# Performance work log

Measured on AMD Instinct MI355X. Metric: run time of the kernel, lower is better.

## Reference

```python
import jax, jax.numpy as jnp
import numpy as np

DIM = 256
WINDOW = 512  # look_backward=1, look_forward=0, causal


def setup_inputs() -> dict:
    key = jax.random.key(0)
    ks = jax.random.split(key, 7)
    B, N, D = 8, 8192, DIM
    s = D ** -0.5
    return {
        "x": jax.random.normal(ks[0], (B, D, N), dtype=jnp.float32),
        "Wq": jax.random.normal(ks[1], (D, D), dtype=jnp.float32) * s,
        "bq": jax.random.normal(ks[2], (D,), dtype=jnp.float32) * 0.01,
        "Wk": jax.random.normal(ks[3], (D, D), dtype=jnp.float32) * s,
        "bk": jax.random.normal(ks[4], (D,), dtype=jnp.float32) * 0.01,
        "Wv": jax.random.normal(ks[5], (D, D), dtype=jnp.float32) * s,
        "bv": jax.random.normal(ks[6], (D,), dtype=jnp.float32) * 0.01,
    }


def _local_attention(q, k, v, window):
    # q,k,v: (B, N, D); causal sliding-window attention, look_backward=1 window.
    b, n, d = q.shape
    nw = n // window  # N assumed multiple of window (autopad no-op here)
    scale = d ** -0.5
    qb = q.reshape(b, nw, window, d)
    kb = k.reshape(b, nw, window, d)
    vb = v.reshape(b, nw, window, d)

    def look_back(t):
        prev = jnp.pad(t, ((0, 0), (1, 0), (0, 0), (0, 0)))[:, :-1]
        return jnp.concatenate([prev, t], axis=2)  # (b, nw, 2*window, d)

    kb2 = look_back(kb)
    vb2 = look_back(vb)

    pos = jnp.arange(n).reshape(nw, window)
    prev_pos = jnp.pad(pos, ((1, 0), (0, 0)), constant_values=-1)[:-1]
    kpos = jnp.concatenate([prev_pos, pos], axis=1)  # (nw, 2*window)
    # causal mask + mask out the (nonexistent) window before window 0
    mask = (pos[:, :, None] >= kpos[:, None, :]) & (kpos[:, None, :] >= 0)

    scores = jnp.einsum('bnqd,bnkd->bnqk', qb, kb2) * scale
    scores = jnp.where(mask[None], scores, jnp.asarray(-1e9, scores.dtype))
    attn = jax.nn.softmax(scores, axis=-1)  # dropout(0.1) omitted: eval mode
    out = jnp.einsum('bnqk,bnkd->bnqd', attn, vb2)
    return out.reshape(b, n, d)


def reference(x, Wq, bq, Wk, bk, Wv, bv):
    # x: (B, D, N) -> permute -> (B, N, D)
    xp = jnp.transpose(x, (0, 2, 1))
    q = xp @ Wq.T + bq
    k = xp @ Wk.T + bk
    v = xp @ Wv.T + bv
    y = xp + _local_attention(q, k, v, WINDOW)  # residual
    return jnp.transpose(y, (0, 2, 1))
```

## Files before the change

kernel.cpp:

```cpp
#include <hip/hip_runtime.h>
#include <hip/hip_bf16.h>

#define DIM  256
#define NSEQ 8192
#define BATCH 8
#define WIN  512

typedef __attribute__((ext_vector_type(8))) short short8;
typedef __attribute__((ext_vector_type(4))) float floatx4;

union PFU { int i[4]; short8 v; };

__device__ __forceinline__ int packbf(float a, float b) {
    __hip_bfloat162 h;
    h.x = __float2bfloat16(a);
    h.y = __float2bfloat16(b);
    int r;
    __builtin_memcpy(&r, &h, 4);
    return r;
}

__global__ __launch_bounds__(256) void k_wcast(const float* __restrict__ w0,
                                               const float* __restrict__ w1,
                                               const float* __restrict__ w2,
                                               __hip_bfloat16* __restrict__ wb) {
    int i = (blockIdx.x * 256 + threadIdx.x) * 4;
    const float* s = (i < 65536) ? (w0 + i) : ((i < 131072) ? (w1 + i - 65536) : (w2 + i - 131072));
    float4 v = *(const float4*)s;
    union { __hip_bfloat16 h[4]; ushort4 u; } cv;
    cv.h[0] = __float2bfloat16(v.x);
    cv.h[1] = __float2bfloat16(v.y);
    cv.h[2] = __float2bfloat16(v.z);
    cv.h[3] = __float2bfloat16(v.w);
    *(ushort4*)(wb + i) = cv.u;
}

__global__ __launch_bounds__(256, 3) void k_prep(const float* __restrict__ x,
                                                 const __hip_bfloat16* __restrict__ wb,
                                                 const float* __restrict__ bq,
                                                 const float* __restrict__ bk,
                                                 const float* __restrict__ bv,
                                                 __hip_bfloat16* __restrict__ qo,
                                                 __hip_bfloat16* __restrict__ ko,
                                                 __hip_bfloat16* __restrict__ vto) {
    __shared__ float ftile[64][68];
    __shared__ __align__(16) char As[32768];
    const int b   = blockIdx.y;
    const int n0  = blockIdx.x * 64;
    const int tid = threadIdx.x;
    const int wv  = tid >> 6;
    const int l   = tid & 63;
    const int lm  = l & 15;
    const int qd  = l >> 4;
    const int wn  = wv * 64;

    const float* xb = x + (size_t)b * DIM * NSEQ;

    const int dr = l >> 4, nseg = l & 15;
#pragma unroll
    for (int dsl = 0; dsl < 4; ++dsl) {
        const int d0 = dsl * 64;
#pragma unroll
        for (int i = 0; i < 4; ++i) {
            const int r = wv * 16 + i * 4 + dr;
            float4 v = *(const float4*)(xb + (size_t)(d0 + r) * NSEQ + n0 + nseg * 4);
            *(float4*)&ftile[r][nseg * 4] = v;
        }
        __syncthreads();
#pragma unroll
        for (int p = 0; p < 2; ++p) {
            const int ks = dsl * 2 + p;
            int4 pk;
            int* pki = (int*)&pk;
#pragma unroll
            for (int jj = 0; jj < 4; ++jj)
                pki[jj] = packbf(ftile[p * 32 + wv * 8 + jj * 2][l],
                                 ftile[p * 32 + wv * 8 + jj * 2 + 1][l]);
            *(int4*)(As + ks * 4096 + wv * 1024 + l * 16) = pk;
        }
        __syncthreads();
    }

#pragma unroll
    for (int mode = 0; mode < 3; ++mode) {
        const __hip_bfloat16* wp = wb + mode * 65536;
        floatx4 acc[4][4];
#pragma unroll
        for (int i = 0; i < 4; ++i)
#pragma unroll
            for (int j = 0; j < 4; ++j) acc[i][j] = (floatx4){0.f, 0.f, 0.f, 0.f};

#pragma unroll
        for (int ks = 0; ks < 8; ++ks) {
            short8 wf[4], af[4];
#pragma unroll
            for (int j = 0; j < 4; ++j)
                wf[j] = *(const short8*)(wp + (size_t)(wn + j * 16 + lm) * DIM + ks * 32 + qd * 8);
#pragma unroll
            for (int j = 0; j < 4; ++j)
                af[j] = *(const short8*)(As + ks * 4096 + qd * 1024 + (j * 16 + lm) * 16);
            if (mode < 2) {
#pragma unroll
                for (int mt = 0; mt < 4; ++mt)
#pragma unroll
                    for (int nt = 0; nt < 4; ++nt)
                        acc[mt][nt] = __builtin_amdgcn_mfma_f32_16x16x32_bf16(af[mt], wf[nt], acc[mt][nt], 0, 0, 0);
            } else {
#pragma unroll
                for (int jw = 0; jw < 4; ++jw)
#pragma unroll
                    for (int ja = 0; ja < 4; ++ja)
                        acc[jw][ja] = __builtin_amdgcn_mfma_f32_16x16x32_bf16(wf[jw], af[ja], acc[jw][ja], 0, 0, 0);
            }
        }

        if (mode < 2) {
            const float* bias = mode ? bk : bq;
            __hip_bfloat16* op = (mode ? ko : qo) + (size_t)b * NSEQ * DIM;
            float bc[4];
#pragma unroll
            for (int nt = 0; nt < 4; ++nt) bc[nt] = bias[wn + nt * 16 + lm];
#pragma unroll
            for (int mt = 0; mt < 4; ++mt)
#pragma unroll
                for (int nt = 0; nt < 4; ++nt)
#pragma unroll
                    for (int r = 0; r < 4; ++r)
                        op[(size_t)(n0 + mt * 16 + qd * 4 + r) * DIM + wn + nt * 16 + lm] =
                            __float2bfloat16(acc[mt][nt][r] + bc[nt]);
        } else {
            __hip_bfloat16* op = vto + (size_t)b * DIM * NSEQ;
#pragma unroll
            for (int jw = 0; jw < 4; ++jw)
#pragma unroll
                for (int r = 0; r < 4; ++r) {
                    const int d = wn + jw * 16 + qd * 4 + r;
                    const float bb = bv[d];
#pragma unroll
                    for (int ja = 0; ja < 4; ++ja)
                        op[(size_t)d * NSEQ + n0 + ja * 16 + lm] =
                            __float2bfloat16(acc[jw][ja][r] + bb);
                }
        }
    }
}

__global__ __launch_bounds__(1024, 4) void k_attn(const __hip_bfloat16* __restrict__ qm,
                                                  const __hip_bfloat16* __restrict__ km,
                                                  const __hip_bfloat16* __restrict__ vtm,
                                                  const float* __restrict__ x,
                                                  float* __restrict__ out) {
    __shared__ __align__(16) char kbuf[2][16384];
    __shared__ __align__(16) char vbuf[2][16384];

    const int w  = blockIdx.x, b = blockIdx.y, qt = blockIdx.z;
    const int tid = threadIdx.x;
    const int wv = tid >> 6;
    const int l  = tid & 63;
    const int m  = l & 15;
    const int qd = l >> 4;

    const int qbw   = qt * 256 + wv * 16;
    const int koff0 = w * WIN - WIN;

    short8 qf[8];
    {
        const __hip_bfloat16* qrow =
            qm + ((size_t)b * NSEQ + (size_t)(w * WIN + qbw + m)) * DIM;
#pragma unroll
        for (int s = 0; s < 8; ++s)
            qf[s] = *(const short8*)(qrow + s * 32 + qd * 8);
    }

    const char* kbase = (const char*)(km + (size_t)b * NSEQ * DIM);
    const char* vbase = (const char*)(vtm + (size_t)b * DIM * NSEQ);

    const int c0  = (w == 0) ? 16 : 0;
    const int c1w = (512 + qbw + 47) >> 5;
    const int c1b = (799 + qt * 256) >> 5;

    const bool   isK = wv < 8;
    const int    wk  = wv & 7;
    const size_t gstride = isK ? (size_t)64 : (size_t)16 * NSEQ * 2;
    const size_t adv     = isK ? (size_t)32 * 512 : (size_t)64;
    const int    lbase   = wk * 2048 + l * 16;
    const char* gp0;
    if (isK)
        gp0 = kbase + (size_t)(koff0 + c0 * 32 + (wk >> 2) * 16 + m) * 512 +
              (size_t)(((wk >> 1) & 1) * 16 + qd) * 16 + (size_t)(wk & 1) * 128;
    else
        gp0 = vbase + (size_t)((wk >> 1) * 64 + (wk & 1) * 32 + m) * (NSEQ * 2) +
              (size_t)(koff0 + c0 * 32) * 2 + (size_t)qd * 16;

    floatx4 o[16];
#pragma unroll
    for (int t = 0; t < 16; ++t) o[t] = (floatx4){0.f, 0.f, 0.f, 0.f};
    float mi = -INFINITY;
    float li = 0.f;
    const float sscale = 0.0625f * 1.4426950408889634f;

    const int a0 = (((qd & 1) * 2) * 16 + m) * 4;
    const int a1 = a0 + 64;
    const bool hi = (qd >> 1) != 0;

    int4 rg[2];
#pragma unroll
    for (int i = 0; i < 2; ++i)
        rg[i] = *(const int4*)(gp0 + (size_t)i * gstride);
    gp0 += adv;
    {
        char* d0 = (isK ? kbuf[0] : vbuf[0]) + lbase;
#pragma unroll
        for (int i = 0; i < 2; ++i)
            *(int4*)(d0 + i * 1024) = rg[i];
    }
    __syncthreads();

    int pb = 0;
    for (int c = c0; c < c1b; ++c) {
        const bool more = (c + 1 < c1b);
        if (more) {
#pragma unroll
            for (int i = 0; i < 2; ++i)
                rg[i] = *(const int4*)(gp0 + (size_t)i * gstride);
            gp0 += adv;
        }
        if (c < c1w) {
            const char* kbp = kbuf[pb];
            floatx4 st[2];
            st[0] = (floatx4){0.f, 0.f, 0.f, 0.f};
            st[1] = (floatx4){0.f, 0.f, 0.f, 0.f};
            __builtin_amdgcn_s_setprio(1);
#pragma unroll
            for (int t = 0; t < 2; ++t)
#pragma unroll
                for (int s = 0; s < 8; ++s) {
                    short8 kf = *(const short8*)(kbp + ((t * 8 + s) * 64 + l) * 16);
                    st[t] = __builtin_amdgcn_mfma_f32_16x16x32_bf16(kf, qf[s], st[t], 0, 0, 0);
                }
            __builtin_amdgcn_s_setprio(0);
            const int kl0 = c * 32;
            const int lim = 512 + qbw + m;
            const bool needmask = (kl0 + 31) > lim;
            float p[8];
#pragma unroll
            for (int t = 0; t < 2; ++t)
#pragma unroll
                for (int r = 0; r < 4; ++r) {
                    float v = st[t][r] * sscale;
                    if (needmask) {
                        int key = kl0 + t * 16 + qd * 4 + r;
                        v = (key <= lim) ? v : -INFINITY;
                    }
                    p[t * 4 + r] = v;
                }
            float mx = p[0];
#pragma unroll
            for (int i = 1; i < 8; ++i) mx = fmaxf(mx, p[i]);
            mx = fmaxf(mx, __shfl_xor(mx, 16, 64));
            mx = fmaxf(mx, __shfl_xor(mx, 32, 64));
            float mnew;
            if (__all(mx <= mi + 8.0f)) mnew = mi;
            else                        mnew = fmaxf(mi, mx);
            const float alpha = exp2f(mi - mnew);
            float ps = 0.f;
#pragma unroll
            for (int i = 0; i < 8; ++i) { p[i] = exp2f(p[i] - mnew); ps += p[i]; }
            ps += __shfl_xor(ps, 16, 64);
            ps += __shfl_xor(ps, 32, 64);
            li = li * alpha + ps;
            mi = mnew;
            if (!__all(alpha == 1.0f)) {
#pragma unroll
                for (int t = 0; t < 16; ++t) {
                    o[t][0] *= alpha; o[t][1] *= alpha;
                    o[t][2] *= alpha; o[t][3] *= alpha;
                }
            }
            int pd0 = packbf(p[0], p[1]);
            int pd1 = packbf(p[2], p[3]);
            int pd2 = packbf(p[4], p[5]);
            int pd3 = packbf(p[6], p[7]);
            int x0 = __builtin_amdgcn_ds_bpermute(a0, pd0);
            int y0 = __builtin_amdgcn_ds_bpermute(a0, pd2);
            int x1 = __builtin_amdgcn_ds_bpermute(a0, pd1);
            int y1 = __builtin_amdgcn_ds_bpermute(a0, pd3);
            int x2 = __builtin_amdgcn_ds_bpermute(a1, pd0);
            int y2 = __builtin_amdgcn_ds_bpermute(a1, pd2);
            int x3 = __builtin_amdgcn_ds_bpermute(a1, pd1);
            int y3 = __builtin_amdgcn_ds_bpermute(a1, pd3);
            PFU pu;
            pu.i[0] = hi ? y0 : x0;
            pu.i[1] = hi ? y1 : x1;
            pu.i[2] = hi ? y2 : x2;
            pu.i[3] = hi ? y3 : x3;
            short8 pf = pu.v;
            const char* vbp = vbuf[pb];
            __builtin_amdgcn_s_setprio(1);
#pragma unroll
            for (int t = 0; t < 16; ++t) {
                short8 vf = *(const short8*)(vbp + (t * 64 + l) * 16);
                o[t] = __builtin_amdgcn_mfma_f32_16x16x32_bf16(vf, pf, o[t], 0, 0, 0);
            }
            __builtin_amdgcn_s_setprio(0);
        }
        if (more) {
            char* dst = (isK ? kbuf[pb ^ 1] : vbuf[pb ^ 1]) + lbase;
#pragma unroll
            for (int i = 0; i < 2; ++i)
                *(int4*)(dst + i * 1024) = rg[i];
        }
        __syncthreads();
        pb ^= 1;
    }

    {
        const float inv = 1.f / li;
        const int ng = w * WIN + qbw + m;
        const float* xr  = x   + (size_t)b * DIM * NSEQ + ng;
        float*       orw = out + (size_t)b * DIM * NSEQ + ng;
#pragma unroll
        for (int t = 0; t < 16; ++t)
#pragma unroll
            for (int r = 0; r < 4; ++r) {
                int d = t * 16 + qd * 4 + r;
                orw[(size_t)d * NSEQ] = xr[(size_t)d * NSEQ] + o[t][r] * inv;
            }
    }
}

extern "C" void kernel_launch(void* const* d_in, const int* in_sizes, int n_in,
                              void* d_out, int out_size, void* d_ws, size_t ws_size,
                              hipStream_t stream) {
    const float* x  = (const float*)d_in[0];
    const float* Wq = (const float*)d_in[1];
    const float* bq = (const float*)d_in[2];
    const float* Wk = (const float*)d_in[3];
    const float* bk = (const float*)d_in[4];
    const float* Wv = (const float*)d_in[5];
    const float* bv = (const float*)d_in[6];

    char* ws = (char*)d_ws;
    const size_t SZ = (size_t)BATCH * NSEQ * DIM * sizeof(__hip_bfloat16);
    __hip_bfloat16* qb_ = (__hip_bfloat16*)(ws);
    __hip_bfloat16* kb_ = (__hip_bfloat16*)(ws + SZ);
    __hip_bfloat16* vt_ = (__hip_bfloat16*)(ws + 2 * SZ);
    __hip_bfloat16* wb_ = (__hip_bfloat16*)(ws + 3 * SZ);

    k_wcast<<<dim3(192), 256, 0, stream>>>(Wq, Wk, Wv, wb_);
    k_prep<<<dim3(NSEQ / 64, BATCH), 256, 0, stream>>>(x, wb_, bq, bk, bv, qb_, kb_, vt_);
    k_attn<<<dim3(16, BATCH, 2), 1024, 0, stream>>>(qb_, kb_, vt_, x, (float*)d_out);
}
```

Measured before the change: 336.1 us.

## Switch attention to 32x32x16 MFMA tiles with swizzled LDS staging

Rewrites the attention kernel so each wave handles 32 query rows using 32x32x16 bf16 MFMA instead of 16x16x32, with 512-thread blocks instead of 1024. K and V tiles are now stored in LDS with an XOR swizzle to avoid bank conflicts. The P-operand reshuffle drops from eight bpermutes to four, and one cross-lane max/sum shuffle step is removed. The aim is fewer LDS reads per FLOP and less shuffle overhead, at the cost of more accumulator registers per wave and fewer waves per block.

```diff
diff --git a/kernel.cpp b/kernel.cpp
--- a/kernel.cpp
+++ b/kernel.cpp
@@ -8,6 +8,7 @@
 
 typedef __attribute__((ext_vector_type(8))) short short8;
 typedef __attribute__((ext_vector_type(4))) float floatx4;
+typedef __attribute__((ext_vector_type(16))) float f32x16;
 
 union PFU { int i[4]; short8 v; };
 
@@ -145,11 +146,11 @@
     }
 }
 
-__global__ __launch_bounds__(1024, 4) void k_attn(const __hip_bfloat16* __restrict__ qm,
-                                                  const __hip_bfloat16* __restrict__ km,
-                                                  const __hip_bfloat16* __restrict__ vtm,
-                                                  const float* __restrict__ x,
-                                                  float* __restrict__ out) {
+__global__ __launch_bounds__(512, 2) void k_attn(const __hip_bfloat16* __restrict__ qm,
+                                                 const __hip_bfloat16* __restrict__ km,
+                                                 const __hip_bfloat16* __restrict__ vtm,
+                                                 const float* __restrict__ x,
+                                                 float* __restrict__ out) {
     __shared__ __align__(16) char kbuf[2][16384];
     __shared__ __align__(16) char vbuf[2][16384];
 
@@ -157,62 +158,69 @@
     const int tid = threadIdx.x;
     const int wv = tid >> 6;
     const int l  = tid & 63;
-    const int m  = l & 15;
-    const int qd = l >> 4;
-
-    const int qbw   = qt * 256 + wv * 16;
+    const int q5 = l & 31;
+    const int hi = l >> 5;
+
+    const int qbw   = qt * 256 + wv * 32;
     const int koff0 = w * WIN - WIN;
 
-    short8 qf[8];
+    short8 qfr[16];
     {
         const __hip_bfloat16* qrow =
-            qm + ((size_t)b * NSEQ + (size_t)(w * WIN + qbw + m)) * DIM;
-#pragma unroll
-        for (int s = 0; s < 8; ++s)
-            qf[s] = *(const short8*)(qrow + s * 32 + qd * 8);
+            qm + ((size_t)b * NSEQ + (size_t)(w * WIN + qbw + q5)) * DIM;
+#pragma unroll
+        for (int s = 0; s < 16; ++s)
+            qfr[s] = *(const short8*)(qrow + s * 16 + hi * 8);
     }
 
     const char* kbase = (const char*)(km + (size_t)b * NSEQ * DIM);
     const char* vbase = (const char*)(vtm + (size_t)b * DIM * NSEQ);
 
     const int c0  = (w == 0) ? 16 : 0;
-    const int c1w = (512 + qbw + 47) >> 5;
+    const int c1w = (575 + qbw) >> 5;
     const int c1b = (799 + qt * 256) >> 5;
 
-    const bool   isK = wv < 8;
-    const int    wk  = wv & 7;
-    const size_t gstride = isK ? (size_t)64 : (size_t)16 * NSEQ * 2;
-    const size_t adv     = isK ? (size_t)32 * 512 : (size_t)64;
-    const int    lbase   = wk * 2048 + l * 16;
+    const bool isK = wv < 4;
     const char* gp0;
-    if (isK)
-        gp0 = kbase + (size_t)(koff0 + c0 * 32 + (wk >> 2) * 16 + m) * 512 +
-              (size_t)(((wk >> 1) & 1) * 16 + qd) * 16 + (size_t)(wk & 1) * 128;
-    else
-        gp0 = vbase + (size_t)((wk >> 1) * 64 + (wk & 1) * 32 + m) * (NSEQ * 2) +
-              (size_t)(koff0 + c0 * 32) * 2 + (size_t)qd * 16;
-
-    floatx4 o[16];
-#pragma unroll
-    for (int t = 0; t < 16; ++t) o[t] = (floatx4){0.f, 0.f, 0.f, 0.f};
+    int lwo[4];
+    size_t adv;
+    if (isK) {
+        const int key = wv * 8 + (l >> 3), seg = l & 7;
+        gp0 = kbase + (size_t)(koff0 + c0 * 32 + key) * 512 + seg * 64;
+        adv = (size_t)32 * 512;
+#pragma unroll
+        for (int j = 0; j < 4; ++j)
+            lwo[j] = key * 512 + (((seg * 4 + j) ^ key) << 4);
+    } else {
+        const int dl = (wv - 4) * 64 + l, dg = dl >> 3, d7 = dl & 7;
+        gp0 = vbase + (size_t)dl * (NSEQ * 2) + (size_t)(koff0 + c0 * 32) * 2;
+        adv = 64;
+#pragma unroll
+        for (int j = 0; j < 4; ++j)
+            lwo[j] = dg * 512 + (((j * 8 + d7) ^ dg) << 4);
+    }
+
+    f32x16 o[8];
+#pragma unroll
+    for (int t = 0; t < 8; ++t)
+#pragma unroll
+        for (int r = 0; r < 16; ++r) o[t][r] = 0.f;
     float mi = -INFINITY;
     float li = 0.f;
     const float sscale = 0.0625f * 1.4426950408889634f;
 
-    const int a0 = (((qd & 1) * 2) * 16 + m) * 4;
-    const int a1 = a0 + 64;
-    const bool hi = (qd >> 1) != 0;
-
-    int4 rg[2];
-#pragma unroll
-    for (int i = 0; i < 2; ++i)
-        rg[i] = *(const int4*)(gp0 + (size_t)i * gstride);
+    const int paddr = (l ^ 32) * 4;
+
+    int4 rg[4];
+#pragma unroll
+    for (int j = 0; j < 4; ++j)
+        rg[j] = *(const int4*)(gp0 + (size_t)j * 16);
     gp0 += adv;
     {
-        char* d0 = (isK ? kbuf[0] : vbuf[0]) + lbase;
-#pragma unroll
-        for (int i = 0; i < 2; ++i)
-            *(int4*)(d0 + i * 1024) = rg[i];
+        char* d0 = (isK ? kbuf[0] : vbuf[0]);
+#pragma unroll
+        for (int j = 0; j < 4; ++j)
+            *(int4*)(d0 + lwo[j]) = rg[j];
     }
     __syncthreads();
 
@@ -221,43 +229,39 @@
         const bool more = (c + 1 < c1b);
         if (more) {
 #pragma unroll
-            for (int i = 0; i < 2; ++i)
-                rg[i] = *(const int4*)(gp0 + (size_t)i * gstride);
+            for (int j = 0; j < 4; ++j)
+                rg[j] = *(const int4*)(gp0 + (size_t)j * 16);
             gp0 += adv;
         }
         if (c < c1w) {
-            const char* kbp = kbuf[pb];
-            floatx4 st[2];
-            st[0] = (floatx4){0.f, 0.f, 0.f, 0.f};
-            st[1] = (floatx4){0.f, 0.f, 0.f, 0.f};
+            const char* kb = kbuf[pb];
+            f32x16 st;
+#pragma unroll
+            for (int r = 0; r < 16; ++r) st[r] = 0.f;
             __builtin_amdgcn_s_setprio(1);
 #pragma unroll
-            for (int t = 0; t < 2; ++t)
-#pragma unroll
-                for (int s = 0; s < 8; ++s) {
-                    short8 kf = *(const short8*)(kbp + ((t * 8 + s) * 64 + l) * 16);
-                    st[t] = __builtin_amdgcn_mfma_f32_16x16x32_bf16(kf, qf[s], st[t], 0, 0, 0);
+            for (int s = 0; s < 16; ++s) {
+                short8 kf = *(const short8*)(kb + q5 * 512 + ((((s * 2 + hi)) ^ q5) << 4));
+                st = __builtin_amdgcn_mfma_f32_32x32x16_bf16(kf, qfr[s], st, 0, 0, 0);
+            }
+            __builtin_amdgcn_s_setprio(0);
+
+            const int kl0 = c * 32;
+            const int lim = 512 + qbw + q5;
+            const bool needmask = (kl0 + 31) > lim;
+            float p[16];
+#pragma unroll
+            for (int r = 0; r < 16; ++r) {
+                float v = st[r] * sscale;
+                if (needmask) {
+                    int k = kl0 + (r & 3) + 8 * (r >> 2) + 4 * hi;
+                    v = (k <= lim) ? v : -INFINITY;
                 }
-            __builtin_amdgcn_s_setprio(0);
-            const int kl0 = c * 32;
-            const int lim = 512 + qbw + m;
-            const bool needmask = (kl0 + 31) > lim;
-            float p[8];
-#pragma unroll
-            for (int t = 0; t < 2; ++t)
-#pragma unroll
-                for (int r = 0; r < 4; ++r) {
-                    float v = st[t][r] * sscale;
-                    if (needmask) {
-                        int key = kl0 + t * 16 + qd * 4 + r;
-                        v = (key <= lim) ? v : -INFINITY;
-                    }
-                    p[t * 4 + r] = v;
-                }
+                p[r] = v;
+            }
             float mx = p[0];
 #pragma unroll
-            for (int i = 1; i < 8; ++i) mx = fmaxf(mx, p[i]);
-            mx = fmaxf(mx, __shfl_xor(mx, 16, 64));
+            for (int r = 1; r < 16; ++r) mx = fmaxf(mx, p[r]);
             mx = fmaxf(mx, __shfl_xor(mx, 32, 64));
             float mnew;
             if (__all(mx <= mi + 8.0f)) mnew = mi;
@@ -265,50 +269,53 @@
             const float alpha = exp2f(mi - mnew);
             float ps = 0.f;
 #pragma unroll
-            for (int i = 0; i < 8; ++i) { p[i] = exp2f(p[i] - mnew); ps += p[i]; }
-            ps += __shfl_xor(ps, 16, 64);
+            for (int r = 0; r < 16; ++r) { p[r] = exp2f(p[r] - mnew); ps += p[r]; }
             ps += __shfl_xor(ps, 32, 64);
             li = li * alpha + ps;
             mi = mnew;
             if (!__all(alpha == 1.0f)) {
 #pragma unroll
-                for (int t = 0; t < 16; ++t) {
-                    o[t][0] *= alpha; o[t][1] *= alpha;
-                    o[t][2] *= alpha; o[t][3] *= alpha;
-                }
-            }
-            int pd0 = packbf(p[0], p[1]);
-            int pd1 = packbf(p[2], p[3]);
-            int pd2 = packbf(p[4], p[5]);
-            int pd3 = packbf(p[6], p[7]);
-            int x0 = __builtin_amdgcn_ds_bpermute(a0, pd0);
-            int y0 = __builtin_amdgcn_ds_bpermute(a0, pd2);
-            int x1 = __builtin_amdgcn_ds_bpermute(a0, pd1);
-            int y1 = __builtin_amdgcn_ds_bpermute(a0, pd3);
-            int x2 = __builtin_amdgcn_ds_bpermute(a1, pd0);
-            int y2 = __builtin_amdgcn_ds_bpermute(a1, pd2);
-            int x3 = __builtin_amdgcn_ds_bpermute(a1, pd1);
-            int y3 = __builtin_amdgcn_ds_bpermute(a1, pd3);
-            PFU pu;
-            pu.i[0] = hi ? y0 : x0;
-            pu.i[1] = hi ? y1 : x1;
-            pu.i[2] = hi ? y2 : x2;
-            pu.i[3] = hi ? y3 : x3;
-            short8 pf = pu.v;
-            const char* vbp = vbuf[pb];
+                for (int t = 0; t < 8; ++t)
+#pragma unroll
+                    for (int r = 0; r < 16; ++r) o[t][r] *= alpha;
+            }
+
+            const int A0 = packbf(p[0], p[1]),  A1 = packbf(p[2], p[3]);
+            const int B0 = packbf(p[4], p[5]),  B1 = packbf(p[6], p[7]);
+            const int C0 = packbf(p[8], p[9]),  C1 = packbf(p[10], p[11]);
+            const int D0 = packbf(p[12], p[13]), D1 = packbf(p[14], p[15]);
+            const int Z0 = hi ? A0 : B0, Z1 = hi ? A1 : B1;
+            const int Z2 = hi ? C0 : D0, Z3 = hi ? C1 : D1;
+            const int P0 = __builtin_amdgcn_ds_bpermute(paddr, Z0);
+            const int P1 = __builtin_amdgcn_ds_bpermute(paddr, Z1);
+            const int P2 = __builtin_amdgcn_ds_bpermute(paddr, Z2);
+            const int P3 = __builtin_amdgcn_ds_bpermute(paddr, Z3);
+            PFU u0, u1;
+            u0.i[0] = hi ? P0 : A0;  u0.i[1] = hi ? P1 : A1;
+            u0.i[2] = hi ? B0 : P0;  u0.i[3] = hi ? B1 : P1;
+            u1.i[0] = hi ? P2 : C0;  u1.i[1] = hi ? P3 : C1;
+            u1.i[2] = hi ? D0 : P2;  u1.i[3] = hi ? D1 : P3;
+            const short8 pf0 = u0.v, pf1 = u1.v;
+
+            const char* vb = vbuf[pb];
+            const int qh = q5 >> 3, d7 = q5 & 7;
+            const int sl0 = hi * 8 + d7, sl1 = 16 + hi * 8 + d7;
             __builtin_amdgcn_s_setprio(1);
 #pragma unroll
-            for (int t = 0; t < 16; ++t) {
-                short8 vf = *(const short8*)(vbp + (t * 64 + l) * 16);
-                o[t] = __builtin_amdgcn_mfma_f32_16x16x32_bf16(vf, pf, o[t], 0, 0, 0);
+            for (int t = 0; t < 8; ++t) {
+                const int dg = t * 4 + qh;
+                short8 vf0 = *(const short8*)(vb + dg * 512 + ((sl0 ^ dg) << 4));
+                o[t] = __builtin_amdgcn_mfma_f32_32x32x16_bf16(vf0, pf0, o[t], 0, 0, 0);
+                short8 vf1 = *(const short8*)(vb + dg * 512 + ((sl1 ^ dg) << 4));
+                o[t] = __builtin_amdgcn_mfma_f32_32x32x16_bf16(vf1, pf1, o[t], 0, 0, 0);
             }
             __builtin_amdgcn_s_setprio(0);
         }
         if (more) {
-            char* dst = (isK ? kbuf[pb ^ 1] : vbuf[pb ^ 1]) + lbase;
-#pragma unroll
-            for (int i = 0; i < 2; ++i)
-                *(int4*)(dst + i * 1024) = rg[i];
+            char* dst = (isK ? kbuf[pb ^ 1] : vbuf[pb ^ 1]);
+#pragma unroll
+            for (int j = 0; j < 4; ++j)
+                *(int4*)(dst + lwo[j]) = rg[j];
         }
         __syncthreads();
         pb ^= 1;
@@ -316,14 +323,14 @@
 
     {
         const float inv = 1.f / li;
-        const int ng = w * WIN + qbw + m;
-        const float* xr  = x   + (size_t)b * DIM * NSEQ + ng;
-        float*       orw = out + (size_t)b * DIM * NSEQ + ng;
-#pragma unroll
-        for (int t = 0; t < 16; ++t)
-#pragma unroll
-            for (int r = 0; r < 4; ++r) {
-                int d = t * 16 + qd * 4 + r;
+        const int n = w * WIN + qbw + q5;
+        const float* xr  = x   + (size_t)b * DIM * NSEQ + n;
+        float*       orw = out + (size_t)b * DIM * NSEQ + n;
+#pragma unroll
+        for (int t = 0; t < 8; ++t)
+#pragma unroll
+            for (int r = 0; r < 16; ++r) {
+                const int d = t * 32 + (r & 3) + 8 * (r >> 2) + 4 * hi;
                 orw[(size_t)d * NSEQ] = xr[(size_t)d * NSEQ] + o[t][r] * inv;
             }
     }
@@ -349,5 +356,5 @@
 
     k_wcast<<<dim3(192), 256, 0, stream>>>(Wq, Wk, Wv, wb_);
     k_prep<<<dim3(NSEQ / 64, BATCH), 256, 0, stream>>>(x, wb_, bq, bk, bv, qb_, kb_, vt_);
-    k_attn<<<dim3(16, BATCH, 2), 1024, 0, stream>>>(qb_, kb_, vt_, x, (float*)d_out);
-}
+    k_attn<<<dim3(16, BATCH, 2), 512, 0, stream>>>(qb_, kb_, vt_, x, (float*)d_out);
+}
```

Result: slower. 431.9 us (+28.5%).
